# Optimization experiments

Hardware: AMD Instinct MI355X
Metric: run time of the kernel (lower is better)

Reference implementation:

```python
import jax, jax.numpy as jnp
import numpy as np

NUM_HEADS = 8

def setup_inputs() -> dict:
    key = jax.random.key(0)
    ks = jax.random.split(key, 7)
    B, N, K, C = 4, 16384, 16, 64
    pcd = jax.random.normal(ks[0], (B, C, N), dtype=jnp.float32)
    neighbors = jax.random.normal(ks[1], (B, C, N, K), dtype=jnp.float32)
    xyz = jax.random.normal(ks[2], (B, 3, N), dtype=jnp.float32)
    idx_all = jax.random.randint(ks[3], (B, N, K), 0, N)
    Wq = jax.random.normal(ks[4], (C, C + 3), dtype=jnp.float32) * 0.1
    Wk = jax.random.normal(ks[5], (C, C + 3), dtype=jnp.float32) * 0.1
    Wv = jax.random.normal(ks[6], (C, C + 3), dtype=jnp.float32) * 0.1
    return {"pcd": pcd, "neighbors": neighbors, "xyz": xyz,
            "Wq": Wq, "Wk": Wk, "Wv": Wv, "idx_all": idx_all}


def reference(pcd, neighbors, xyz, Wq, Wk, Wv, idx_all):
    B, C, N = pcd.shape
    K = neighbors.shape[-1]
    H = NUM_HEADS
    D = C // H
    # --- query: concat xyz, 1x1 conv, split heads ---
    pcd_cat = jnp.concatenate([pcd, xyz], axis=1)                 # (B, C+3, N)
    q = jnp.einsum('oc,bcn->bon', Wq, pcd_cat)                    # (B, C, N)
    q = q.reshape(B, H, D, N).transpose(0, 1, 3, 2)               # (B, H, N, D)
    # --- index_points: gather xyz at KNN indices (irregular gather) ---
    xyz_t = xyz.transpose(0, 2, 1)                                # (B, N, 3)
    rel_xyz = jax.vmap(lambda pts, ix: pts[ix])(xyz_t, idx_all)   # (B, N, K, 3)
    nb = jnp.concatenate([neighbors, rel_xyz.transpose(0, 3, 1, 2)], axis=1)  # (B, C+3, N, K)
    # --- key/value: 1x1 conv + split heads ---
    k = jnp.einsum('oc,bcnk->bonk', Wk, nb).reshape(B, H, D, N, K).transpose(0, 1, 3, 4, 2)  # (B,H,N,K,D)
    v = jnp.einsum('oc,bcnk->bonk', Wv, nb).reshape(B, H, D, N, K).transpose(0, 1, 3, 4, 2)  # (B,H,N,K,D)
    # --- local scalar-dot attention over the K neighbors of each point ---
    energy = jnp.einsum('bhnd,bhnkd->bhnk', q, k) / jnp.sqrt(jnp.float32(D))  # (B,H,N,K)
    attn = jax.nn.softmax(energy, axis=-1)
    x = jnp.einsum('bhnk,bhnkd->bhnd', attn, v)                   # (B, H, N, D)
    # (B,H,N,D) -> (B,N,H*D) -> (B, C, N), matching torch reshape/permute order
    out = x.transpose(0, 2, 1, 3).reshape(B, N, H * D).transpose(0, 2, 1)
    return out
```

## Files before the change

kernel.cpp:

```cpp
#include <hip/hip_runtime.h>
#include <math.h>

#define B_ 4
#define C_ 64
#define N_ 16384
#define K_ 16
#define H_ 8
#define CP 67
#define CPAD 68
#define NP 16
#define ESTRIDE 552
#define WSZ (C_ * CPAD)

__device__ __align__(16) float wpad[3 * WSZ];

__global__ void setup_weights(const float* __restrict__ Wq,
                              const float* __restrict__ Wk,
                              const float* __restrict__ Wv) {
  int i = blockIdx.x * blockDim.x + threadIdx.x;
  if (i >= WSZ) return;
  int j = i >> 6, o = i & 63;
  float q = 0.f, kk = 0.f, v = 0.f;
  if (j < CP) {
    q = Wq[o * CP + j] * 0.35355339059327373f;
    kk = Wk[o * CP + j];
    v = Wv[o * CP + j];
  }
  wpad[i] = q;
  wpad[WSZ + i] = kk;
  wpad[2 * WSZ + i] = v;
}

#define SWZ(v, imm) __int_as_float(__builtin_amdgcn_ds_swizzle(__float_as_int(v), (imm)))
#define XOR4 0x101F

#define DPP_XOR1 0xB1
#define DPP_XOR2 0x4E
#define DPP_ROR4 0x124
#define DPP_ROR8 0x128
template <int CTRL>
__device__ __forceinline__ float dppf(float x) {
  int i = __float_as_int(x);
  return __int_as_float(__builtin_amdgcn_update_dpp(i, i, CTRL, 0xF, 0xF, false));
}

__launch_bounds__(256, 4)
__global__ void pt_attn(const float* __restrict__ pcd,
                        const float* __restrict__ neighbors,
                        const float* __restrict__ xyz,
                        const int* __restrict__ idx_all,
                        float* __restrict__ out) {
  __shared__ __align__(16) float x_lds[NP * CPAD];
  __shared__ __align__(16) float e_lds[NP * ESTRIDE];

  const int tid = threadIdx.x;
  const int p = tid >> 4;
  const int k = tid & 15;
  const int blk = blockIdx.x;
  const int b = blk >> 10;
  const int n0 = (blk & 1023) << 4;
  const int n = n0 + p;

  float nb[CPAD];
  {
    const float* gp = neighbors + (size_t)b * (C_ * N_ * K_) + n0 * K_ + tid;
#pragma unroll
    for (int c = 0; c < C_; ++c)
      nb[c] = gp[(size_t)c * (N_ * K_)];
  }
  {
    const int idx = idx_all[(b * N_ + n) * K_ + k];
    const float* gx = xyz + (size_t)b * (3 * N_) + idx;
    nb[64] = gx[0];
    nb[65] = gx[N_];
    nb[66] = gx[2 * N_];
    nb[67] = 0.f;
  }

  {
    const int pp = tid & 15;
    const int c0 = tid >> 4;
#pragma unroll
    for (int it = 0; it < 4; ++it) {
      int c = c0 + it * 16;
      x_lds[pp * CPAD + c] = pcd[((size_t)b * C_ + c) * N_ + n0 + pp];
    }
    if (tid < 48)
      x_lds[pp * CPAD + 64 + c0] = xyz[((size_t)b * 3 + c0) * N_ + n0 + pp];
    if (tid < 16)
      x_lds[pp * CPAD + 67] = 0.f;
  }
  __syncthreads();

  const int h = k & 7;
  float a0 = 0.f, a1 = 0.f, a2 = 0.f, a3 = 0.f;
  {
    const float4* xr = (const float4*)(x_lds + p * CPAD);
    const float* wq = wpad + 8 * h + 4 * (k >> 3);
#pragma unroll
    for (int j4 = 0; j4 < 17; ++j4) {
      float4 xv = xr[j4];
      float4 w0 = *(const float4*)(wq + (4 * j4 + 0) * 64);
      float4 w1 = *(const float4*)(wq + (4 * j4 + 1) * 64);
      float4 w2 = *(const float4*)(wq + (4 * j4 + 2) * 64);
      float4 w3 = *(const float4*)(wq + (4 * j4 + 3) * 64);
      a0 += w0.x * xv.x + w1.x * xv.y + w2.x * xv.z + w3.x * xv.w;
      a1 += w0.y * xv.x + w1.y * xv.y + w2.y * xv.z + w3.y * xv.w;
      a2 += w0.z * xv.x + w1.z * xv.y + w2.z * xv.z + w3.z * xv.w;
      a3 += w0.w * xv.x + w1.w * xv.y + w2.w * xv.z + w3.w * xv.w;
    }
  }

  {
    float b0 = dppf<DPP_ROR8>(a0);
    float b1 = dppf<DPP_ROR8>(a1);
    float b2 = dppf<DPP_ROR8>(a2);
    float b3 = dppf<DPP_ROR8>(a3);
    const bool hi = (k & 8) != 0;
    float qa0 = hi ? b0 : a0, qa1 = hi ? b1 : a1;
    float qa2 = hi ? b2 : a2, qa3 = hi ? b3 : a3;
    float qa4 = hi ? a0 : b0, qa5 = hi ? a1 : b1;
    float qa6 = hi ? a2 : b2, qa7 = hi ? a3 : b3;

    const float* wk = wpad + WSZ + 8 * h;
    float4* er = (float4*)(e_lds + p * ESTRIDE + h * CPAD);
    const int jb = (k >> 3) * 8;
#pragma unroll
    for (int u = 0; u < 9; ++u) {
      int j4 = jb + u;
      float r[4];
#pragma unroll
      for (int jj = 0; jj < 4; ++jj) {
        const float4 wlo = *(const float4*)(wk + (4 * j4 + jj) * 64);
        const float4 whi = *(const float4*)(wk + (4 * j4 + jj) * 64 + 4);
        r[jj] = qa0 * wlo.x + qa1 * wlo.y + qa2 * wlo.z + qa3 * wlo.w +
                qa4 * whi.x + qa5 * whi.y + qa6 * whi.z + qa7 * whi.w;
      }
      er[j4] = make_float4(r[0], r[1], r[2], r[3]);
    }
  }
  asm volatile("s_waitcnt lgkmcnt(0)" ::: "memory");
  __builtin_amdgcn_sched_barrier(0);

  float en[8];
#pragma unroll
  for (int hh = 0; hh < 8; ++hh) en[hh] = 0.f;
  {
    const float4* ep = (const float4*)(e_lds + p * ESTRIDE);
#pragma unroll
    for (int j4 = 0; j4 < 17; ++j4) {
#pragma unroll
      for (int hh = 0; hh < 8; ++hh) {
        float4 e4 = ep[hh * 17 + j4];
        en[hh] += e4.x * nb[4 * j4 + 0] + e4.y * nb[4 * j4 + 1] +
                  e4.z * nb[4 * j4 + 2] + e4.w * nb[4 * j4 + 3];
      }
    }
  }
  float at[8];
#pragma unroll
  for (int hh = 0; hh < 8; ++hh) {
    float m = en[hh];
    m = fmaxf(m, dppf<DPP_XOR1>(m));
    m = fmaxf(m, dppf<DPP_XOR2>(m));
    m = fmaxf(m, dppf<DPP_ROR4>(m));
    m = fmaxf(m, dppf<DPP_ROR8>(m));
    float e = __expf(en[hh] - m);
    float s = e;
    s += dppf<DPP_XOR1>(s);
    s += dppf<DPP_XOR2>(s);
    s += dppf<DPP_ROR4>(s);
    s += dppf<DPP_ROR8>(s);
    at[hh] = e * __builtin_amdgcn_rcpf(s);
  }

  const int g = (((k >> 3) & 1) << 2) | (((k >> 1) & 1) << 1) | (k & 1);
  float ap[8];
  {
    float t0[8], t1[8];
#pragma unroll
    for (int i = 0; i < 8; ++i) t0[i] = (k & 8) ? at[i ^ 4] : at[i];
#pragma unroll
    for (int i = 0; i < 8; ++i) t1[i] = (k & 2) ? t0[i ^ 2] : t0[i];
#pragma unroll
    for (int i = 0; i < 8; ++i) ap[i] = (k & 1) ? t1[i ^ 1] : t1[i];
  }

  const int ob = 8 * g + (k & 4);
  float xo0 = 0.f, xo1 = 0.f, xo2 = 0.f, xo3 = 0.f;
  {
    const float* wv = wpad + 2 * WSZ + ob;
#pragma unroll
    for (int j4 = 0; j4 < 17; ++j4) {
      float agg0, agg1, agg2, agg3;
#pragma unroll
      for (int u = 0; u < 4; ++u) {
        float nbj = nb[4 * j4 + u];
        float s0 = ap[0] * nbj, s1 = ap[1] * nbj, s2 = ap[2] * nbj, s3 = ap[3] * nbj;
        float s4 = ap[4] * nbj, s5 = ap[5] * nbj, s6 = ap[6] * nbj, s7 = ap[7] * nbj;
        s0 += dppf<DPP_ROR8>(s4);
        s1 += dppf<DPP_ROR8>(s5);
        s2 += dppf<DPP_ROR8>(s6);
        s3 += dppf<DPP_ROR8>(s7);
        s0 += dppf<DPP_XOR2>(s2);
        s1 += dppf<DPP_XOR2>(s3);
        s0 += dppf<DPP_XOR1>(s1);
        s0 += SWZ(s0, XOR4);
        if (u == 0) agg0 = s0;
        else if (u == 1) agg1 = s0;
        else if (u == 2) agg2 = s0;
        else agg3 = s0;
      }
      float4 w0 = *(const float4*)(wv + (4 * j4 + 0) * 64);
      float4 w1 = *(const float4*)(wv + (4 * j4 + 1) * 64);
      float4 w2 = *(const float4*)(wv + (4 * j4 + 2) * 64);
      float4 w3 = *(const float4*)(wv + (4 * j4 + 3) * 64);
      xo0 += w0.x * agg0 + w1.x * agg1 + w2.x * agg2 + w3.x * agg3;
      xo1 += w0.y * agg0 + w1.y * agg1 + w2.y * agg2 + w3.y * agg3;
      xo2 += w0.z * agg0 + w1.z * agg1 + w2.z * agg2 + w3.z * agg3;
      xo3 += w0.w * agg0 + w1.w * agg1 + w2.w * agg2 + w3.w * agg3;
    }
  }

  __syncthreads();
  {
    float* ol = x_lds;
    ol[(ob + 0) * 17 + p] = xo0;
    ol[(ob + 1) * 17 + p] = xo1;
    ol[(ob + 2) * 17 + p] = xo2;
    ol[(ob + 3) * 17 + p] = xo3;
  }
  __syncthreads();
  {
    const int o = tid >> 2;
    const int pc = (tid & 3) << 2;
    const float* ol = x_lds + o * 17 + pc;
    float4 vo = make_float4(ol[0], ol[1], ol[2], ol[3]);
    *(float4*)(out + ((size_t)b * C_ + o) * N_ + n0 + pc) = vo;
  }
}

extern "C" void kernel_launch(void* const* d_in, const int* in_sizes, int n_in,
                              void* d_out, int out_size, void* d_ws, size_t ws_size,
                              hipStream_t stream) {
  const float* pcd = (const float*)d_in[0];
  const float* neighbors = (const float*)d_in[1];
  const float* xyz = (const float*)d_in[2];
  const float* Wq = (const float*)d_in[3];
  const float* Wk = (const float*)d_in[4];
  const float* Wv = (const float*)d_in[5];
  const int* idx = (const int*)d_in[6];
  float* out = (float*)d_out;

  setup_weights<<<(WSZ + 255) / 256, 256, 0, stream>>>(Wq, Wk, Wv);
  pt_attn<<<B_ * (N_ / NP), 256, 0, stream>>>(pcd, neighbors, xyz, idx, out);
}
```

Baseline: 680.5 us.

## Split channel reduction across two lanes per neighbor, halving points per block

Each block now handles 8 points instead of 16, with two 16-lane halves per point that each hold half of the 67 neighbor channels. Partial sums for the query projection, energies and the value output are combined with an XOR-16 swizzle. This cuts per-thread registers from about 68 neighbor values to 36, aiming at higher occupancy and more loads in flight. In exchange it adds cross-lane reductions, launches twice as many blocks, redoes the query projection work, and writes output with narrower float2 stores.

```diff
diff --git a/kernel.cpp b/kernel.cpp
--- a/kernel.cpp
+++ b/kernel.cpp
@@ -8,8 +8,9 @@
 #define H_ 8
 #define CP 67
 #define CPAD 68
-#define NP 16
+#define NP 8
 #define ESTRIDE 552
+#define TSTRIDE 9
 #define WSZ (C_ * CPAD)
 
 __device__ __align__(16) float wpad[3 * WSZ];
@@ -33,6 +34,7 @@
 
 #define SWZ(v, imm) __int_as_float(__builtin_amdgcn_ds_swizzle(__float_as_int(v), (imm)))
 #define XOR4 0x101F
+#define XOR16 0x401F
 
 #define DPP_XOR1 0xB1
 #define DPP_XOR2 0x4E
@@ -50,93 +52,119 @@
                         const float* __restrict__ xyz,
                         const int* __restrict__ idx_all,
                         float* __restrict__ out) {
-  __shared__ __align__(16) float x_lds[NP * CPAD];
+  __shared__ __align__(16) float x_lds[640];
   __shared__ __align__(16) float e_lds[NP * ESTRIDE];
 
   const int tid = threadIdx.x;
-  const int p = tid >> 4;
   const int k = tid & 15;
+  const int s = (tid >> 4) & 1;
+  const int p = tid >> 5;
   const int blk = blockIdx.x;
-  const int b = blk >> 10;
-  const int n0 = (blk & 1023) << 4;
+  const int b = blk >> 11;
+  const int n0 = (blk & 2047) << 3;
   const int n = n0 + p;
 
-  float nb[CPAD];
-  {
-    const float* gp = neighbors + (size_t)b * (C_ * N_ * K_) + n0 * K_ + tid;
-#pragma unroll
-    for (int c = 0; c < C_; ++c)
-      nb[c] = gp[(size_t)c * (N_ * K_)];
-  }
-  {
+  float nbr[36];
+  {
+    const float* gp = neighbors + (size_t)b * (C_ * N_ * K_) +
+                      (size_t)(n0 + p) * K_ + k + (size_t)s * 4 * (N_ * K_);
+#pragma unroll
+    for (int t = 0; t < 8; ++t)
+#pragma unroll
+      for (int u = 0; u < 4; ++u)
+        nbr[4 * t + u] = gp[(size_t)(8 * t + u) * (N_ * K_)];
+  }
+  if (s == 0) {
     const int idx = idx_all[(b * N_ + n) * K_ + k];
     const float* gx = xyz + (size_t)b * (3 * N_) + idx;
-    nb[64] = gx[0];
-    nb[65] = gx[N_];
-    nb[66] = gx[2 * N_];
-    nb[67] = 0.f;
-  }
-
-  {
-    const int pp = tid & 15;
-    const int c0 = tid >> 4;
-#pragma unroll
-    for (int it = 0; it < 4; ++it) {
-      int c = c0 + it * 16;
+    nbr[32] = gx[0];
+    nbr[33] = gx[N_];
+    nbr[34] = gx[2 * N_];
+    nbr[35] = 0.f;
+  }
+
+  {
+    const int pp = tid & 7;
+    const int cc = tid >> 3;
+#pragma unroll
+    for (int it = 0; it < 2; ++it) {
+      int c = cc + 32 * it;
       x_lds[pp * CPAD + c] = pcd[((size_t)b * C_ + c) * N_ + n0 + pp];
     }
-    if (tid < 48)
-      x_lds[pp * CPAD + 64 + c0] = xyz[((size_t)b * 3 + c0) * N_ + n0 + pp];
-    if (tid < 16)
-      x_lds[pp * CPAD + 67] = 0.f;
+    if (tid < 24)
+      x_lds[pp * CPAD + 64 + cc] = xyz[((size_t)b * 3 + cc) * N_ + n0 + pp];
+    if (tid < 8)
+      x_lds[tid * CPAD + 67] = 0.f;
   }
   __syncthreads();
 
-  const int h = k & 7;
-  float a0 = 0.f, a1 = 0.f, a2 = 0.f, a3 = 0.f;
+  float4 q4;
   {
     const float4* xr = (const float4*)(x_lds + p * CPAD);
-    const float* wq = wpad + 8 * h + 4 * (k >> 3);
-#pragma unroll
-    for (int j4 = 0; j4 < 17; ++j4) {
+    const float* wq = wpad + 4 * k;
+    float ax = 0.f, ay = 0.f, az = 0.f, aw = 0.f;
+#pragma unroll
+    for (int t = 0; t < 8; ++t) {
+      const int j4 = 2 * t + s;
       float4 xv = xr[j4];
-      float4 w0 = *(const float4*)(wq + (4 * j4 + 0) * 64);
-      float4 w1 = *(const float4*)(wq + (4 * j4 + 1) * 64);
-      float4 w2 = *(const float4*)(wq + (4 * j4 + 2) * 64);
-      float4 w3 = *(const float4*)(wq + (4 * j4 + 3) * 64);
-      a0 += w0.x * xv.x + w1.x * xv.y + w2.x * xv.z + w3.x * xv.w;
-      a1 += w0.y * xv.x + w1.y * xv.y + w2.y * xv.z + w3.y * xv.w;
-      a2 += w0.z * xv.x + w1.z * xv.y + w2.z * xv.z + w3.z * xv.w;
-      a3 += w0.w * xv.x + w1.w * xv.y + w2.w * xv.z + w3.w * xv.w;
-    }
-  }
-
-  {
-    float b0 = dppf<DPP_ROR8>(a0);
-    float b1 = dppf<DPP_ROR8>(a1);
-    float b2 = dppf<DPP_ROR8>(a2);
-    float b3 = dppf<DPP_ROR8>(a3);
-    const bool hi = (k & 8) != 0;
-    float qa0 = hi ? b0 : a0, qa1 = hi ? b1 : a1;
-    float qa2 = hi ? b2 : a2, qa3 = hi ? b3 : a3;
-    float qa4 = hi ? a0 : b0, qa5 = hi ? a1 : b1;
-    float qa6 = hi ? a2 : b2, qa7 = hi ? a3 : b3;
-
+#pragma unroll
+      for (int jj = 0; jj < 4; ++jj) {
+        float4 w = *(const float4*)(wq + (4 * j4 + jj) * 64);
+        float xc = (jj == 0) ? xv.x : (jj == 1) ? xv.y : (jj == 2) ? xv.z : xv.w;
+        ax += w.x * xc; ay += w.y * xc; az += w.z * xc; aw += w.w * xc;
+      }
+    }
+    if (s == 0) {
+      float4 xv = xr[16];
+#pragma unroll
+      for (int jj = 0; jj < 4; ++jj) {
+        float4 w = *(const float4*)(wq + (64 + jj) * 64);
+        float xc = (jj == 0) ? xv.x : (jj == 1) ? xv.y : (jj == 2) ? xv.z : xv.w;
+        ax += w.x * xc; ay += w.y * xc; az += w.z * xc; aw += w.w * xc;
+      }
+    }
+    ax += SWZ(ax, XOR16);
+    ay += SWZ(ay, XOR16);
+    az += SWZ(az, XOR16);
+    aw += SWZ(aw, XOR16);
+    q4 = make_float4(ax, ay, az, aw);
+  }
+
+  {
+    float bx = dppf<DPP_XOR1>(q4.x), by = dppf<DPP_XOR1>(q4.y);
+    float bz = dppf<DPP_XOR1>(q4.z), bw = dppf<DPP_XOR1>(q4.w);
+    const bool lo = (k & 1) == 0;
+    const float qa0 = lo ? q4.x : bx, qa1 = lo ? q4.y : by;
+    const float qa2 = lo ? q4.z : bz, qa3 = lo ? q4.w : bw;
+    const float qa4 = lo ? bx : q4.x, qa5 = lo ? by : q4.y;
+    const float qa6 = lo ? bz : q4.z, qa7 = lo ? bw : q4.w;
+    const int h = k >> 1;
+    const int idx4 = (k & 1) * 2 + s;
     const float* wk = wpad + WSZ + 8 * h;
     float4* er = (float4*)(e_lds + p * ESTRIDE + h * CPAD);
-    const int jb = (k >> 3) * 8;
-#pragma unroll
-    for (int u = 0; u < 9; ++u) {
-      int j4 = jb + u;
+#pragma unroll
+    for (int t = 0; t < 4; ++t) {
+      const int j4 = idx4 + 4 * t;
       float r[4];
 #pragma unroll
       for (int jj = 0; jj < 4; ++jj) {
-        const float4 wlo = *(const float4*)(wk + (4 * j4 + jj) * 64);
-        const float4 whi = *(const float4*)(wk + (4 * j4 + jj) * 64 + 4);
-        r[jj] = qa0 * wlo.x + qa1 * wlo.y + qa2 * wlo.z + qa3 * wlo.w +
-                qa4 * whi.x + qa5 * whi.y + qa6 * whi.z + qa7 * whi.w;
+        const float4 wl = *(const float4*)(wk + (4 * j4 + jj) * 64);
+        const float4 wh = *(const float4*)(wk + (4 * j4 + jj) * 64 + 4);
+        r[jj] = qa0 * wl.x + qa1 * wl.y + qa2 * wl.z + qa3 * wl.w +
+                qa4 * wh.x + qa5 * wh.y + qa6 * wh.z + qa7 * wh.w;
       }
       er[j4] = make_float4(r[0], r[1], r[2], r[3]);
+    }
+    if (idx4 == 0) {
+      float r[4];
+#pragma unroll
+      for (int jj = 0; jj < 4; ++jj) {
+        const float4 wl = *(const float4*)(wk + (64 + jj) * 64);
+        const float4 wh = *(const float4*)(wk + (64 + jj) * 64 + 4);
+        r[jj] = qa0 * wl.x + qa1 * wl.y + qa2 * wl.z + qa3 * wl.w +
+                qa4 * wh.x + qa5 * wh.y + qa6 * wh.z + qa7 * wh.w;
+      }
+      er[16] = make_float4(r[0], r[1], r[2], r[3]);
     }
   }
   asm volatile("s_waitcnt lgkmcnt(0)" ::: "memory");
@@ -148,30 +176,39 @@
   {
     const float4* ep = (const float4*)(e_lds + p * ESTRIDE);
 #pragma unroll
-    for (int j4 = 0; j4 < 17; ++j4) {
+    for (int t = 0; t < 8; ++t) {
+      const int j4 = 2 * t + s;
 #pragma unroll
       for (int hh = 0; hh < 8; ++hh) {
         float4 e4 = ep[hh * 17 + j4];
-        en[hh] += e4.x * nb[4 * j4 + 0] + e4.y * nb[4 * j4 + 1] +
-                  e4.z * nb[4 * j4 + 2] + e4.w * nb[4 * j4 + 3];
+        en[hh] += e4.x * nbr[4 * t + 0] + e4.y * nbr[4 * t + 1] +
+                  e4.z * nbr[4 * t + 2] + e4.w * nbr[4 * t + 3];
+      }
+    }
+    if (s == 0) {
+#pragma unroll
+      for (int hh = 0; hh < 8; ++hh) {
+        float4 e4 = ep[hh * 17 + 16];
+        en[hh] += e4.x * nbr[32] + e4.y * nbr[33] + e4.z * nbr[34] + e4.w * nbr[35];
       }
     }
   }
   float at[8];
 #pragma unroll
   for (int hh = 0; hh < 8; ++hh) {
-    float m = en[hh];
+    float e0 = en[hh] + SWZ(en[hh], XOR16);
+    float m = e0;
     m = fmaxf(m, dppf<DPP_XOR1>(m));
     m = fmaxf(m, dppf<DPP_XOR2>(m));
     m = fmaxf(m, dppf<DPP_ROR4>(m));
     m = fmaxf(m, dppf<DPP_ROR8>(m));
-    float e = __expf(en[hh] - m);
-    float s = e;
-    s += dppf<DPP_XOR1>(s);
-    s += dppf<DPP_XOR2>(s);
-    s += dppf<DPP_ROR4>(s);
-    s += dppf<DPP_ROR8>(s);
-    at[hh] = e * __builtin_amdgcn_rcpf(s);
+    float e = __expf(e0 - m);
+    float sum = e;
+    sum += dppf<DPP_XOR1>(sum);
+    sum += dppf<DPP_XOR2>(sum);
+    sum += dppf<DPP_ROR4>(sum);
+    sum += dppf<DPP_ROR8>(sum);
+    at[hh] = e * __builtin_amdgcn_rcpf(sum);
   }
 
   const int g = (((k >> 3) & 1) << 2) | (((k >> 1) & 1) << 1) | (k & 1);
@@ -188,55 +225,64 @@
 
   const int ob = 8 * g + (k & 4);
   float xo0 = 0.f, xo1 = 0.f, xo2 = 0.f, xo3 = 0.f;
-  {
-    const float* wv = wpad + 2 * WSZ + ob;
-#pragma unroll
-    for (int j4 = 0; j4 < 17; ++j4) {
-      float agg0, agg1, agg2, agg3;
-#pragma unroll
-      for (int u = 0; u < 4; ++u) {
-        float nbj = nb[4 * j4 + u];
-        float s0 = ap[0] * nbj, s1 = ap[1] * nbj, s2 = ap[2] * nbj, s3 = ap[3] * nbj;
-        float s4 = ap[4] * nbj, s5 = ap[5] * nbj, s6 = ap[6] * nbj, s7 = ap[7] * nbj;
-        s0 += dppf<DPP_ROR8>(s4);
-        s1 += dppf<DPP_ROR8>(s5);
-        s2 += dppf<DPP_ROR8>(s6);
-        s3 += dppf<DPP_ROR8>(s7);
-        s0 += dppf<DPP_XOR2>(s2);
-        s1 += dppf<DPP_XOR2>(s3);
-        s0 += dppf<DPP_XOR1>(s1);
-        s0 += SWZ(s0, XOR4);
-        if (u == 0) agg0 = s0;
-        else if (u == 1) agg1 = s0;
-        else if (u == 2) agg2 = s0;
-        else agg3 = s0;
-      }
-      float4 w0 = *(const float4*)(wv + (4 * j4 + 0) * 64);
-      float4 w1 = *(const float4*)(wv + (4 * j4 + 1) * 64);
-      float4 w2 = *(const float4*)(wv + (4 * j4 + 2) * 64);
-      float4 w3 = *(const float4*)(wv + (4 * j4 + 3) * 64);
-      xo0 += w0.x * agg0 + w1.x * agg1 + w2.x * agg2 + w3.x * agg3;
-      xo1 += w0.y * agg0 + w1.y * agg1 + w2.y * agg2 + w3.y * agg3;
-      xo2 += w0.z * agg0 + w1.z * agg1 + w2.z * agg2 + w3.z * agg3;
-      xo3 += w0.w * agg0 + w1.w * agg1 + w2.w * agg2 + w3.w * agg3;
-    }
-  }
+  const float* wv = wpad + 2 * WSZ + ob;
+
+#define PH4_GROUP(M, ROWB)                                                   \
+  {                                                                          \
+    float agg0, agg1, agg2, agg3;                                            \
+    _Pragma("unroll") for (int u = 0; u < 4; ++u) {                          \
+      float nbj = nbr[4 * (M) + u];                                          \
+      float s0 = ap[0] * nbj, s1 = ap[1] * nbj, s2 = ap[2] * nbj,            \
+            s3 = ap[3] * nbj;                                                \
+      float s4 = ap[4] * nbj, s5 = ap[5] * nbj, s6 = ap[6] * nbj,            \
+            s7 = ap[7] * nbj;                                                \
+      s0 += dppf<DPP_ROR8>(s4);                                              \
+      s1 += dppf<DPP_ROR8>(s5);                                              \
+      s2 += dppf<DPP_ROR8>(s6);                                              \
+      s3 += dppf<DPP_ROR8>(s7);                                              \
+      s0 += dppf<DPP_XOR2>(s2);                                              \
+      s1 += dppf<DPP_XOR2>(s3);                                              \
+      s0 += dppf<DPP_XOR1>(s1);                                              \
+      s0 += SWZ(s0, XOR4);                                                   \
+      if (u == 0) agg0 = s0;                                                 \
+      else if (u == 1) agg1 = s0;                                            \
+      else if (u == 2) agg2 = s0;                                            \
+      else agg3 = s0;                                                        \
+    }                                                                        \
+    float4 w0 = *(const float4*)(wv + ((ROWB) + 0) * 64);                    \
+    float4 w1 = *(const float4*)(wv + ((ROWB) + 1) * 64);                    \
+    float4 w2 = *(const float4*)(wv + ((ROWB) + 2) * 64);                    \
+    float4 w3 = *(const float4*)(wv + ((ROWB) + 3) * 64);                    \
+    xo0 += w0.x * agg0 + w1.x * agg1 + w2.x * agg2 + w3.x * agg3;            \
+    xo1 += w0.y * agg0 + w1.y * agg1 + w2.y * agg2 + w3.y * agg3;            \
+    xo2 += w0.z * agg0 + w1.z * agg1 + w2.z * agg2 + w3.z * agg3;            \
+    xo3 += w0.w * agg0 + w1.w * agg1 + w2.w * agg2 + w3.w * agg3;            \
+  }
+
+#pragma unroll
+  for (int t = 0; t < 8; ++t) {
+    PH4_GROUP(t, 4 * (2 * t + s));
+  }
+  if (s == 0) {
+    PH4_GROUP(8, 64);
+  }
+  xo0 += SWZ(xo0, XOR16);
+  xo1 += SWZ(xo1, XOR16);
+  xo2 += SWZ(xo2, XOR16);
+  xo3 += SWZ(xo3, XOR16);
 
   __syncthreads();
   {
-    float* ol = x_lds;
-    ol[(ob + 0) * 17 + p] = xo0;
-    ol[(ob + 1) * 17 + p] = xo1;
-    ol[(ob + 2) * 17 + p] = xo2;
-    ol[(ob + 3) * 17 + p] = xo3;
+    const int oo = ob + 2 * s;
+    x_lds[(oo + 0) * TSTRIDE + p] = s ? xo2 : xo0;
+    x_lds[(oo + 1) * TSTRIDE + p] = s ? xo3 : xo1;
   }
   __syncthreads();
   {
     const int o = tid >> 2;
-    const int pc = (tid & 3) << 2;
-    const float* ol = x_lds + o * 17 + pc;
-    float4 vo = make_float4(ol[0], ol[1], ol[2], ol[3]);
-    *(float4*)(out + ((size_t)b * C_ + o) * N_ + n0 + pc) = vo;
+    const int pc = (tid & 3) << 1;
+    const float* ol = x_lds + o * TSTRIDE + pc;
+    *(float2*)(out + ((size_t)b * C_ + o) * N_ + n0 + pc) = make_float2(ol[0], ol[1]);
   }
 }
 
```

Measured after the change: 861.8 us. +26.6%, slower.
